# Optimization experiments

Measured on AMD Instinct MI355X. Metric: run time of the kernel, lower is better.

Reference implementation:

```python
import jax, jax.numpy as jnp
import numpy as np

D = 300   # hidden dim (Linear(300,300))
L = 160   # seq len, forced by W3 = Linear(160,1)


def _linear(x, W, b):
    # torch Linear: x @ W.T + b, W is (out, in)
    return jnp.matmul(x, W.T) + b


def setup_inputs() -> dict:
    key = jax.random.key(0)
    ks = jax.random.split(key, 16)
    B = 1024
    s = 1.0 / np.sqrt(D)
    inp = {
        'T_feature': jax.random.normal(ks[0], (B, L, D), jnp.float32),
        'CD_feature': jax.random.normal(ks[1], (B, L, D), jnp.float32),
        'Wproj': jax.random.normal(ks[2], (D, D), jnp.float32) * s,
        'bproj': jnp.zeros((D,), jnp.float32),
        'WqT_w': jax.random.normal(ks[3], (D, D), jnp.float32) * s,
        'WqT_b': jnp.zeros((D,), jnp.float32),
        'WqCD_w': jax.random.normal(ks[4], (D, D), jnp.float32) * s,
        'WqCD_b': jnp.zeros((D,), jnp.float32),
        'WkT_w': jax.random.normal(ks[5], (D, D), jnp.float32) * s,
        'WkT_b': jnp.zeros((D,), jnp.float32),
        'WkCD_w': jax.random.normal(ks[6], (D, D), jnp.float32) * s,
        'WkCD_b': jnp.zeros((D,), jnp.float32),
        'W3_w': jax.random.normal(ks[7], (1, L), jnp.float32) * (1.0 / np.sqrt(L)),
        'W3_b': jnp.zeros((1,), jnp.float32),
    }
    return inp


def reference(T_feature, CD_feature, Wproj, bproj, WqT_w, WqT_b, WqCD_w, WqCD_b,
              WkT_w, WkT_b, WkCD_w, WkCD_b, W3_w, W3_b):
    sqrt_d = jnp.sqrt(jnp.float32(D))
    proj_T = _linear(T_feature, Wproj, bproj)     # (B, L, D)
    proj_CD = _linear(CD_feature, Wproj, bproj)   # (B, L, D)

    # N_tensor @ proj_T is just the mean over tokens (weights 1/Len)
    mean_T = jnp.mean(proj_T, axis=1, keepdims=True)          # (B, 1, D)
    qT = _linear(mean_T, WqT_w, WqT_b)                        # (B, 1, D)
    kT = _linear(proj_T, WkT_w, WkT_b)                        # (B, L, D)
    alphaT = jnp.einsum('bqd,bkd->bqk', qT, kT) / sqrt_d      # (B, 1, L)
    ZT = jax.nn.sigmoid(alphaT)

    qCD = _linear(proj_CD, WqCD_w, WqCD_b)                    # (B, L, D)
    kCD = _linear(proj_CD, WkCD_w, WkCD_b)                    # (B, L, D)
    alphaCD = jnp.einsum('bqd,bkd->bqk', qCD, kCD) / sqrt_d   # (B, L, L)
    ZCD = jax.nn.sigmoid(alphaCD)

    # The per-token loop+cat is a plain broadcast multiply: Mt[:,i,:] = ZCD[:,i,:] * ZT[:,0,:]
    Mt = ZCD * ZT                                             # (B, L, L)
    alpha_f = jax.nn.softmax(_linear(Mt, W3_w, W3_b), axis=1) # (B, L, 1)

    # Second loop is a per-token scalar scale: HCD[:,i,:] = alpha_f[:,i,0] * proj_CD[:,i,:]
    HCD = alpha_f * proj_CD                                   # (B, L, D)
    return (proj_T, HCD)
```

## Files before the change

kernel.cpp:

```cpp
#include <hip/hip_runtime.h>
#include <hip/hip_bf16.h>


typedef __attribute__((ext_vector_type(8))) short short8;
typedef __attribute__((ext_vector_type(4))) float f32x4;

#define DP 320

__device__ __forceinline__ unsigned short f2bf(float x) {
  unsigned int u = __builtin_bit_cast(unsigned int, x);
  u += 0x7FFFu + ((u >> 16) & 1u);
  return (unsigned short)(u >> 16);
}
__device__ __forceinline__ float bf2f(unsigned short h) {
  unsigned int u = ((unsigned int)h) << 16;
  return __builtin_bit_cast(float, u);
}
__device__ __forceinline__ void gload16(const void* g, void* l) {
  __builtin_amdgcn_global_load_lds(
      (const __attribute__((address_space(1))) unsigned int*)g,
      (__attribute__((address_space(3))) unsigned int*)l, 16, 0, 0);
}
__device__ __forceinline__ float sigm(float x) { return 1.0f / (1.0f + __expf(-x)); }
__device__ __forceinline__ size_t baddr(int n, int k) {
  return (size_t)(k >> 6) * 20480 + (size_t)(n >> 4) * 1024 + ((k >> 5) & 1) * 512 +
         ((((k >> 3) & 3) << 4) | (n & 15)) * 8 + (k & 7);
}
__device__ __forceinline__ size_t aaddr(size_t r, int k) {
  return ((r >> 4) * 5 + (k >> 6)) * 1024 + ((k >> 5) & 1) * 512 +
         ((((k >> 3) & 3) << 4) | (r & 15)) * 8 + (k & 7);
}

__global__ __launch_bounds__(320)
void prep1_k(const float* __restrict__ W,
             const float* __restrict__ WqCD_w, const float* __restrict__ WqCD_b,
             const float* __restrict__ WkCD_w, const float* __restrict__ WkCD_b,
             const float* __restrict__ WqT_w, const float* __restrict__ WqT_b,
             const float* __restrict__ WkT_w, const float* __restrict__ WkT_b,
             unsigned short* __restrict__ Wb, float* __restrict__ Wt,
             unsigned short* __restrict__ MaugT, float* __restrict__ Maug_f,
             float* __restrict__ Pmat, float isd) {
  const int x = blockIdx.x, c = threadIdx.x;
  if (x < 320) {
    const int n = x;
    unsigned short v = (n < 300 && c < 300) ? f2bf(W[n * 300 + c]) : (unsigned short)0;
    Wb[baddr(n, c)] = v;
    if (n < 300 && c < 300) Wt[c * 304 + n] = W[n * 300 + c];
  } else if (x < 640) {
    const int n = x - 320;
    float v = 0.f;
    if (n <= 300 && c <= 300) {
      for (int o = 0; o < 300; ++o) {
        float a = (c < 300) ? WqCD_w[o * 300 + c] : WqCD_b[o];
        float b = (n < 300) ? WkCD_w[o * 300 + n] : WkCD_b[o];
        v += a * b;
      }
      v *= isd;
    }
    MaugT[baddr(n, c)] = f2bf(v);
    Maug_f[n * DP + c] = v;
  } else {
    const int n = x - 640;
    float v = 0.f;
    if (n <= 300 && c <= 300) {
      for (int o = 0; o < 300; ++o) {
        float a = (c < 300) ? WkT_w[o * 300 + c] : WkT_b[o];
        float b = (n < 300) ? WqT_w[o * 300 + n] : WqT_b[o];
        v += a * b;
      }
      v *= isd;
    }
    Pmat[n * DP + c] = v;
  }
}

__global__ __launch_bounds__(320)
void gh_k(const float* __restrict__ Maug_f, const float* __restrict__ W,
          const float* __restrict__ bproj, unsigned short* __restrict__ Gswz,
          float* __restrict__ h) {
  const int n = blockIdx.x, o = threadIdx.x;
  float v = 0.f;
  if (o < 300) {
    for (int c = 0; c < 300; ++c) v += Maug_f[n * DP + c] * W[c * 300 + o];
  } else if (o == 300) {
    float s = 0.f;
    for (int c = 0; c < 300; ++c) s += Maug_f[n * DP + c] * bproj[c];
    h[n] = s + Maug_f[n * DP + 300];
  }
  if (o > 300 && o == 301) {  }
  Gswz[baddr(n, o)] = (o < 300) ? f2bf(v) : (unsigned short)0;
  if (o == 300 && n == 0) {  }
}

__global__ __launch_bounds__(256)
void cvt_k(const float* __restrict__ T, const float* __restrict__ CD,
           unsigned short* __restrict__ Abf) {
  unsigned idx = blockIdx.x * 256 + threadIdx.x;
  if (idx >= 20480u * 640u) return;
  unsigned row16 = idx / 640u, rem = idx - row16 * 640u;
  int kc = rem >> 7, kk = (rem >> 6) & 1, lane = rem & 63;
  int lr = lane & 15, hi = lane >> 4;
  size_t row = (size_t)row16 * 16 + lr;
  int col0 = kc * 64 + kk * 32 + hi * 8;
  const float* base = (row < 163840u) ? T + row * 300 : CD + (row - 163840u) * 300;
  short8 h;
  if (col0 + 8 <= 300) {
    f32x4 x0 = *(const f32x4*)(base + col0), x1 = *(const f32x4*)(base + col0 + 4);
#pragma unroll
    for (int j = 0; j < 4; ++j) { h[j] = (short)f2bf(x0[j]); h[j + 4] = (short)f2bf(x1[j]); }
  } else {
#pragma unroll
    for (int j = 0; j < 8; ++j) {
      int c = col0 + j;
      h[j] = (short)((c < 300) ? f2bf(base[c]) : (unsigned short)0);
    }
  }
  *(short8*)(Abf + (size_t)idx * 8) = h;
}

__global__ __launch_bounds__(256, 2)
void gemm_k(const unsigned short* __restrict__ A0, const unsigned short* __restrict__ A1,
            const unsigned short* __restrict__ A2,
            const unsigned short* __restrict__ B01, const unsigned short* __restrict__ B2,
            const float* __restrict__ bias, const float* __restrict__ ybias,
            float* __restrict__ Of, unsigned short* __restrict__ pCDout,
            unsigned short* __restrict__ Yout, int mode_base) {
  __shared__ __align__(16) unsigned short Bs[2][20480];
  const int tid = threadIdx.x, wid = tid >> 6, lane = tid & 63;
  const int lr = lane & 15, hi = lane >> 4;
  const int mode = mode_base + blockIdx.y;
  const unsigned short* __restrict__ A = (mode == 0) ? A0 : (mode == 1) ? A1 : A2;
  const unsigned short* __restrict__ Bm = (mode == 2) ? B2 : B01;
  const size_t m0 = (size_t)blockIdx.x * 128;
  const size_t rt0 = (m0 >> 4) + wid * 2;

  f32x4 acc[2][20];
#pragma unroll
  for (int i = 0; i < 2; ++i)
#pragma unroll
    for (int j = 0; j < 20; ++j) acc[i][j] = (f32x4){0.f, 0.f, 0.f, 0.f};

  auto stageB = [&](int buf, int kc) {
#pragma unroll
    for (int it = 0; it < 10; ++it) {
      int idx = it * 256 + tid;
      gload16(Bm + (size_t)kc * 20480 + (size_t)idx * 8, (char*)Bs[buf] + idx * 16);
    }
  };
  short8 af[2][2][2];
  auto loadA = [&](short8 (&dst)[2][2], int kc) {
#pragma unroll
    for (int mf = 0; mf < 2; ++mf)
#pragma unroll
      for (int kk = 0; kk < 2; ++kk)
        dst[mf][kk] = *(const short8*)(A + ((rt0 + mf) * 5 + kc) * 1024 + kk * 512 + lane * 8);
  };

  stageB(0, 0);
  loadA(af[0], 0);
  __syncthreads();
#pragma unroll
  for (int kc = 0; kc < 5; ++kc) {
    const int cur = kc & 1;
    if (kc < 4) { stageB(cur ^ 1, kc + 1); loadA(af[cur ^ 1], kc + 1); }
#pragma unroll
    for (int kk = 0; kk < 2; ++kk)
#pragma unroll
      for (int nf = 0; nf < 20; ++nf) {
        short8 bb = *(const short8*)&Bs[cur][nf * 1024 + kk * 512 + lane * 8];
#pragma unroll
        for (int mf = 0; mf < 2; ++mf)
          acc[mf][nf] = __builtin_amdgcn_mfma_f32_16x16x32_bf16(af[cur][mf][kk], bb, acc[mf][nf], 0, 0, 0);
      }
    __syncthreads();
  }

#pragma unroll
  for (int mf = 0; mf < 2; ++mf)
#pragma unroll
    for (int nf = 0; nf < 20; ++nf) {
      const int col = nf * 16 + lr;
      const float bv = (mode == 2) ? (ybias ? ybias[col] : 0.f)
                                   : ((col < 300) ? bias[col] : 0.f);
      const size_t row16o = rt0 + mf;
#pragma unroll
      for (int r = 0; r < 4; ++r) {
        const size_t row = (row16o << 4) + hi * 4 + r;
        float v = acc[mf][nf][r] + bv;
        if (mode == 0) {
          if (col < 300) Of[row * 300 + col] = v;
        } else {
          unsigned short u = (mode == 2) ? f2bf(v)
                           : (col < 300) ? f2bf(v)
                           : (col == 300) ? f2bf(1.0f) : (unsigned short)0;
          unsigned short* dst = (mode == 1) ? pCDout : Yout;
          dst[(row16o * 5 + (col >> 6)) * 1024 + ((col >> 5) & 1) * 512 +
              ((((col >> 3) & 3) << 4) | (hi * 4 + r)) * 8 + (col & 7)] = u;
        }
      }
    }
}

__global__ __launch_bounds__(320)
void gate2_k(const float* __restrict__ T, const float* __restrict__ Pmat,
             const float* __restrict__ W, const float* __restrict__ Wt,
             const float* __restrict__ bproj, float* __restrict__ ZT) {
  __shared__ float mt[304];
  __shared__ float maug[304];
  __shared__ float vv[304];
  __shared__ float wt[304];
  __shared__ float cpr;
  const int b = blockIdx.x, t = threadIdx.x;
  const int wid = t >> 6, lane = t & 63;
  const float* Tb = T + (size_t)b * 48000;
  if (t < 300) {
    float s = 0.f;
#pragma unroll 4
    for (int l = 0; l < 160; ++l) s += Tb[l * 300 + t];
    mt[t] = s * (1.0f / 160.0f);
  }
  __syncthreads();
  if (t < 304) {
    if (t < 300) {
      float s = 0.f;
      for (int o = 0; o < 300; ++o) s += Wt[o * 304 + t] * mt[o];
      maug[t] = s + bproj[t];
    } else maug[t] = (t == 300) ? 1.f : 0.f;
  }
  __syncthreads();
  if (t < 304) {
    float s = 0.f;
    if (t <= 300) for (int a = 0; a <= 300; ++a) s += Pmat[a * DP + t] * maug[a];
    vv[t] = s;
  }
  __syncthreads();
  if (t < 304) {
    if (t < 300) {
      float s = 0.f;
      for (int c = 0; c < 300; ++c) s += vv[c] * W[c * 300 + t];
      wt[t] = s;
    } else {
      wt[t] = 0.f;
      if (t == 300) {
        float s = 0.f;
        for (int c = 0; c < 300; ++c) s += vv[c] * bproj[c];
        cpr = s + vv[300];
      }
    }
  }
  __syncthreads();
  for (int j = wid * 32; j < wid * 32 + 32; ++j) {
    const float* row = Tb + j * 300;
    float s = 0.f;
    for (int c = lane; c < 300; c += 64) s += wt[c] * row[c];
#pragma unroll
    for (int m = 1; m < 64; m <<= 1) s += __shfl_xor(s, m, 64);
    if (lane == 0) ZT[b * 160 + j] = sigm(s + cpr);
  }
}

__global__ __launch_bounds__(640)
void finale_k(const unsigned short* __restrict__ Yg, const unsigned short* __restrict__ Pg,
              const float* __restrict__ ZT, const float* __restrict__ W3w,
              float* __restrict__ out) {
  __shared__ __align__(16) unsigned short Ps[51200];
  __shared__ float t_arr[160];
  __shared__ float s_arr[160];
  __shared__ float red0;
  const int b = blockIdx.x, tid = threadIdx.x, wid = tid >> 6, lane = tid & 63;
  const int lr = lane & 15, hi = lane >> 4;
  const unsigned short* Pb = Pg + (size_t)b * 51200;
  const unsigned short* Yb = Yg + (size_t)b * 51200;

  if (tid < 160) t_arr[tid] = ZT[b * 160 + tid] * W3w[tid];

  auto stageP = [&](int kc) {
#pragma unroll
    for (int it = 0; it < 2; ++it) {
      int idx = it * 640 + tid;
      int r16 = idx >> 7, rem = idx & 127;
      gload16(Pb + ((size_t)r16 * 5 + kc) * 1024 + (size_t)rem * 8,
              (char*)Ps + ((size_t)kc * 10240 + (size_t)idx * 8) * 2);
    }
  };
  short8 yf[2][2];
  auto loadY = [&](short8 (&dst)[2], int kc) {
#pragma unroll
    for (int kk = 0; kk < 2; ++kk)
      dst[kk] = *(const short8*)(Yb + ((size_t)wid * 5 + kc) * 1024 + kk * 512 + lane * 8);
  };

  f32x4 acc[10];
#pragma unroll
  for (int j = 0; j < 10; ++j) acc[j] = (f32x4){0.f, 0.f, 0.f, 0.f};

  stageP(0);
  loadY(yf[0], 0);
  __syncthreads();
#pragma unroll
  for (int kc = 0; kc < 5; ++kc) {
    const int cur = kc & 1;
    if (kc < 4) { stageP(kc + 1); loadY(yf[cur ^ 1], kc + 1); }
#pragma unroll
    for (int kk = 0; kk < 2; ++kk)
#pragma unroll
      for (int nf = 0; nf < 10; ++nf) {
        short8 bb = *(const short8*)&Ps[kc * 10240 + nf * 1024 + kk * 512 + lane * 8];
        acc[nf] = __builtin_amdgcn_mfma_f32_16x16x32_bf16(yf[cur][kk], bb, acc[nf], 0, 0, 0);
      }
    __syncthreads();
  }

  float pp[4];
#pragma unroll
  for (int r = 0; r < 4; ++r) {
    float s = 0.f;
#pragma unroll
    for (int nf = 0; nf < 10; ++nf) s += sigm(acc[nf][r]) * t_arr[nf * 16 + lr];
    pp[r] = s;
  }
#pragma unroll
  for (int m = 1; m < 16; m <<= 1)
#pragma unroll
    for (int r = 0; r < 4; ++r) pp[r] += __shfl_xor(pp[r], m, 64);
  if (lr == 0) {
#pragma unroll
    for (int r = 0; r < 4; ++r) s_arr[wid * 16 + hi * 4 + r] = pp[r];
  }
  __syncthreads();
  if (wid == 0) {
    float v0 = s_arr[lane], v1 = s_arr[lane + 64];
    float v2 = (lane < 32) ? s_arr[lane + 128] : -3.0e38f;
    float mx = fmaxf(fmaxf(v0, v1), v2);
#pragma unroll
    for (int m = 1; m < 64; m <<= 1) mx = fmaxf(mx, __shfl_xor(mx, m, 64));
    float e0 = __expf(v0 - mx), e1 = __expf(v1 - mx);
    float e2 = (lane < 32) ? __expf(v2 - mx) : 0.f;
    s_arr[lane] = e0; s_arr[lane + 64] = e1;
    if (lane < 32) s_arr[lane + 128] = e2;
    float sm = e0 + e1 + e2;
#pragma unroll
    for (int m = 1; m < 64; m <<= 1) sm += __shfl_xor(sm, m, 64);
    if (lane == 0) red0 = 1.0f / sm;
  }
  __syncthreads();
  const float inv = red0;
  float* ob = out + (size_t)b * 48000;
#pragma unroll
  for (int it = 0; it < 10; ++it) {
    int idx = it * 640 + tid;
    int i = idx / 40, g = idx - i * 40;
    int c0 = g * 8;
    if (c0 < 300) {
      short8 pv = *(const short8*)&Ps[(g >> 3) * 10240 + (i >> 4) * 1024 +
                                      ((g >> 2) & 1) * 512 + ((((g & 3) << 4) | (i & 15)) * 8)];
      float sc = s_arr[i] * inv;
      if (c0 + 8 <= 300) {
        f32x4 o0, o1;
#pragma unroll
        for (int j = 0; j < 4; ++j) { o0[j] = sc * bf2f((unsigned short)pv[j]); o1[j] = sc * bf2f((unsigned short)pv[j + 4]); }
        *(f32x4*)(ob + (size_t)i * 300 + c0) = o0;
        *(f32x4*)(ob + (size_t)i * 300 + c0 + 4) = o1;
      } else {
#pragma unroll
        for (int j = 0; j < 8; ++j) {
          int c = c0 + j;
          if (c < 300) ob[(size_t)i * 300 + c] = sc * bf2f((unsigned short)pv[j]);
        }
      }
    }
  }
}

extern "C" void kernel_launch(void* const* d_in, const int* in_sizes, int n_in,
                              void* d_out, int out_size, void* d_ws, size_t ws_size,
                              hipStream_t stream) {
  (void)in_sizes; (void)n_in; (void)out_size;
  const float* T      = (const float*)d_in[0];
  const float* CD     = (const float*)d_in[1];
  const float* Wproj  = (const float*)d_in[2];
  const float* bproj  = (const float*)d_in[3];
  const float* WqT_w  = (const float*)d_in[4];
  const float* WqT_b  = (const float*)d_in[5];
  const float* WqCD_w = (const float*)d_in[6];
  const float* WqCD_b = (const float*)d_in[7];
  const float* WkT_w  = (const float*)d_in[8];
  const float* WkT_b  = (const float*)d_in[9];
  const float* WkCD_w = (const float*)d_in[10];
  const float* WkCD_b = (const float*)d_in[11];
  const float* W3_w   = (const float*)d_in[12];

  char* ws = (char*)d_ws;
  size_t off = 0;
  auto alloc = [&](size_t bytes) { void* p = ws + off; off = (off + bytes + 255) & ~(size_t)255; return p; };
  unsigned short* Wb     = (unsigned short*)alloc((size_t)DP * DP * 2);
  unsigned short* MaugT  = (unsigned short*)alloc((size_t)DP * DP * 2);
  unsigned short* Gswz   = (unsigned short*)alloc((size_t)DP * DP * 2);
  float* Maug_f = (float*)alloc((size_t)DP * DP * 4);
  float* Pmat   = (float*)alloc((size_t)DP * DP * 4);
  float* Wt     = (float*)alloc((size_t)304 * 304 * 4);
  float* hb     = (float*)alloc((size_t)DP * 4);
  float* ZT     = (float*)alloc((size_t)1024 * 160 * 4);
  unsigned short* Abf = (unsigned short*)alloc((size_t)327680 * DP * 2);
  unsigned short* AbfCD = Abf + (size_t)163840 * DP;

  const size_t half = (size_t)163840 * DP * 2;
  const bool big = (ws_size > off) && ((ws_size - off) >= 2 * half + 1024);
  unsigned short* pCDg = big ? (unsigned short*)alloc(half) : AbfCD;
  unsigned short* Yg   = big ? (unsigned short*)alloc(half) : Abf;

  float* projT = (float*)d_out;
  float* HCD   = (float*)d_out + (size_t)49152000;

  const float isd = 1.0f / sqrtf(300.0f);

  prep1_k<<<dim3(960), dim3(320), 0, stream>>>(Wproj, WqCD_w, WqCD_b, WkCD_w, WkCD_b,
                                               WqT_w, WqT_b, WkT_w, WkT_b,
                                               Wb, Wt, MaugT, Maug_f, Pmat, isd);
  gh_k<<<dim3(320), dim3(320), 0, stream>>>(Maug_f, Wproj, bproj, Gswz, hb);
  cvt_k<<<dim3(51200), dim3(256), 0, stream>>>(T, CD, Abf);
  gate2_k<<<dim3(1024), dim3(320), 0, stream>>>(T, Pmat, Wproj, Wt, bproj, ZT);

  if (big) {
    gemm_k<<<dim3(1280, 3), dim3(256), 0, stream>>>(Abf, AbfCD, AbfCD, Wb, Gswz,
                                                    bproj, hb, projT, pCDg, Yg, 0);
  } else {
    gemm_k<<<dim3(1280, 2), dim3(256), 0, stream>>>(Abf, AbfCD, nullptr, Wb, nullptr,
                                                    bproj, nullptr, projT, pCDg, nullptr, 0);
    gemm_k<<<dim3(1280, 1), dim3(256), 0, stream>>>(nullptr, nullptr, pCDg, Wb, MaugT,
                                                    bproj, nullptr, projT, nullptr, Yg, 2);
  }
  finale_k<<<dim3(1024), dim3(640), 0, stream>>>(Yg, pCDg, ZT, W3_w, HCD);
}
```

Before: 688.8 us.

## Fuse fp32-to-bf16 conversion into GEMM and retile to 512-thread 2D warp grid

Removes the separate cvt_k pass that wrote a bf16 swizzled copy of T and CD, and the gh_k kernel. The GEMM now loads fp32 rows directly, converts them to bf16 in registers and writes them into a double-buffered LDS A tile. The GEMM also moves from 256 threads with 2x20 fragments per warp to 512 threads in a 2x4 warp grid with 4x5 fragments. The Y GEMM is always run in a second pass from pCD with MaugT, and the gh_k/Gswz shortcut is dropped. This removes a large bf16 write and read round trip, at the cost of more in-kernel conversion and an extra dependent launch.

```diff
diff --git a/kernel.cpp b/kernel.cpp
--- a/kernel.cpp
+++ b/kernel.cpp
@@ -38,8 +38,8 @@
              const float* __restrict__ WqT_w, const float* __restrict__ WqT_b,
              const float* __restrict__ WkT_w, const float* __restrict__ WkT_b,
              unsigned short* __restrict__ Wb, float* __restrict__ Wt,
-             unsigned short* __restrict__ MaugT, float* __restrict__ Maug_f,
-             float* __restrict__ Pmat, float isd) {
+             unsigned short* __restrict__ MaugT, float* __restrict__ Pmat,
+             float isd) {
   const int x = blockIdx.x, c = threadIdx.x;
   if (x < 320) {
     const int n = x;
@@ -58,7 +58,6 @@
       v *= isd;
     }
     MaugT[baddr(n, c)] = f2bf(v);
-    Maug_f[n * DP + c] = v;
   } else {
     const int n = x - 640;
     float v = 0.f;
@@ -74,131 +73,134 @@
   }
 }
 
-__global__ __launch_bounds__(320)
-void gh_k(const float* __restrict__ Maug_f, const float* __restrict__ W,
-          const float* __restrict__ bproj, unsigned short* __restrict__ Gswz,
-          float* __restrict__ h) {
-  const int n = blockIdx.x, o = threadIdx.x;
-  float v = 0.f;
-  if (o < 300) {
-    for (int c = 0; c < 300; ++c) v += Maug_f[n * DP + c] * W[c * 300 + o];
-  } else if (o == 300) {
-    float s = 0.f;
-    for (int c = 0; c < 300; ++c) s += Maug_f[n * DP + c] * bproj[c];
-    h[n] = s + Maug_f[n * DP + 300];
-  }
-  if (o > 300 && o == 301) {  }
-  Gswz[baddr(n, o)] = (o < 300) ? f2bf(v) : (unsigned short)0;
-  if (o == 300 && n == 0) {  }
-}
-
-__global__ __launch_bounds__(256)
-void cvt_k(const float* __restrict__ T, const float* __restrict__ CD,
-           unsigned short* __restrict__ Abf) {
-  unsigned idx = blockIdx.x * 256 + threadIdx.x;
-  if (idx >= 20480u * 640u) return;
-  unsigned row16 = idx / 640u, rem = idx - row16 * 640u;
-  int kc = rem >> 7, kk = (rem >> 6) & 1, lane = rem & 63;
-  int lr = lane & 15, hi = lane >> 4;
-  size_t row = (size_t)row16 * 16 + lr;
-  int col0 = kc * 64 + kk * 32 + hi * 8;
-  const float* base = (row < 163840u) ? T + row * 300 : CD + (row - 163840u) * 300;
-  short8 h;
-  if (col0 + 8 <= 300) {
-    f32x4 x0 = *(const f32x4*)(base + col0), x1 = *(const f32x4*)(base + col0 + 4);
-#pragma unroll
-    for (int j = 0; j < 4; ++j) { h[j] = (short)f2bf(x0[j]); h[j + 4] = (short)f2bf(x1[j]); }
-  } else {
-#pragma unroll
-    for (int j = 0; j < 8; ++j) {
-      int c = col0 + j;
-      h[j] = (short)((c < 300) ? f2bf(base[c]) : (unsigned short)0);
-    }
-  }
-  *(short8*)(Abf + (size_t)idx * 8) = h;
-}
-
-__global__ __launch_bounds__(256, 2)
-void gemm_k(const unsigned short* __restrict__ A0, const unsigned short* __restrict__ A1,
-            const unsigned short* __restrict__ A2,
-            const unsigned short* __restrict__ B01, const unsigned short* __restrict__ B2,
-            const float* __restrict__ bias, const float* __restrict__ ybias,
+__global__ __launch_bounds__(512)
+void gemm_k(const float* __restrict__ Tf, const float* __restrict__ CDf,
+            const unsigned short* __restrict__ Ah,
+            const unsigned short* __restrict__ B01,
+            const unsigned short* __restrict__ B2,
+            const float* __restrict__ bias,
             float* __restrict__ Of, unsigned short* __restrict__ pCDout,
             unsigned short* __restrict__ Yout, int mode_base) {
+  __shared__ __align__(16) unsigned short As[2][8192];
   __shared__ __align__(16) unsigned short Bs[2][20480];
   const int tid = threadIdx.x, wid = tid >> 6, lane = tid & 63;
   const int lr = lane & 15, hi = lane >> 4;
+  const int wr = wid >> 2, wc = wid & 3;
   const int mode = mode_base + blockIdx.y;
-  const unsigned short* __restrict__ A = (mode == 0) ? A0 : (mode == 1) ? A1 : A2;
+  const size_t m0 = (size_t)blockIdx.x * 128;
   const unsigned short* __restrict__ Bm = (mode == 2) ? B2 : B01;
-  const size_t m0 = (size_t)blockIdx.x * 128;
-  const size_t rt0 = (m0 >> 4) + wid * 2;
-
-  f32x4 acc[2][20];
-#pragma unroll
-  for (int i = 0; i < 2; ++i)
-#pragma unroll
-    for (int j = 0; j < 20; ++j) acc[i][j] = (f32x4){0.f, 0.f, 0.f, 0.f};
-
+  const float* __restrict__ Af = (mode == 0) ? Tf : CDf;
+
+  f32x4 acc[4][5];
+#pragma unroll
+  for (int i = 0; i < 4; ++i)
+#pragma unroll
+    for (int j = 0; j < 5; ++j) acc[i][j] = (f32x4){0.f, 0.f, 0.f, 0.f};
+
+  f32x4 ar[4];
+  auto loadA = [&](int kc) {
+#pragma unroll
+    for (int u = 0; u < 2; ++u) {
+      const int unit = tid * 2 + u;
+      const int row = unit >> 3, cg = unit & 7;
+      const int col0 = kc * 64 + cg * 8;
+      const float* p = Af + (m0 + row) * 300 + col0;
+      if (col0 + 8 <= 300) {
+        ar[u * 2] = *(const f32x4*)p;
+        ar[u * 2 + 1] = *(const f32x4*)(p + 4);
+      } else {
+#pragma unroll
+        for (int j = 0; j < 4; ++j) {
+          ar[u * 2][j] = (col0 + j < 300) ? p[j] : 0.f;
+          ar[u * 2 + 1][j] = (col0 + 4 + j < 300) ? p[4 + j] : 0.f;
+        }
+      }
+    }
+  };
+  auto writeA = [&](int buf) {
+#pragma unroll
+    for (int u = 0; u < 2; ++u) {
+      const int unit = tid * 2 + u;
+      const int row = unit >> 3, cg = unit & 7;
+      short8 h;
+#pragma unroll
+      for (int j = 0; j < 4; ++j) {
+        h[j] = (short)f2bf(ar[u * 2][j]);
+        h[j + 4] = (short)f2bf(ar[u * 2 + 1][j]);
+      }
+      *(short8*)&As[buf][(size_t)(row >> 4) * 1024 + (size_t)(cg >> 2) * 512 +
+                         ((((cg & 3) << 4) | (row & 15)) * 8)] = h;
+    }
+  };
+  auto stageA2 = [&](int buf, int kc) {
+#pragma unroll
+    for (int it = 0; it < 2; ++it) {
+      int idx = it * 512 + tid;
+      gload16(Ah + (((m0 >> 4) + (idx >> 7)) * 5 + kc) * 1024 + (size_t)(idx & 127) * 8,
+              (char*)As[buf] + (size_t)idx * 16);
+    }
+  };
   auto stageB = [&](int buf, int kc) {
 #pragma unroll
-    for (int it = 0; it < 10; ++it) {
-      int idx = it * 256 + tid;
-      gload16(Bm + (size_t)kc * 20480 + (size_t)idx * 8, (char*)Bs[buf] + idx * 16);
-    }
-  };
-  short8 af[2][2][2];
-  auto loadA = [&](short8 (&dst)[2][2], int kc) {
-#pragma unroll
-    for (int mf = 0; mf < 2; ++mf)
-#pragma unroll
-      for (int kk = 0; kk < 2; ++kk)
-        dst[mf][kk] = *(const short8*)(A + ((rt0 + mf) * 5 + kc) * 1024 + kk * 512 + lane * 8);
-  };
-
-  stageB(0, 0);
-  loadA(af[0], 0);
-  __syncthreads();
-#pragma unroll
+    for (int it = 0; it < 5; ++it) {
+      int idx = it * 512 + tid;
+      gload16(Bm + (size_t)kc * 20480 + (size_t)idx * 8, (char*)Bs[buf] + (size_t)idx * 16);
+    }
+  };
+
+  if (mode < 2) { loadA(0); stageB(0, 0); writeA(0); }
+  else { stageA2(0, 0); stageB(0, 0); }
+  __syncthreads();
+
   for (int kc = 0; kc < 5; ++kc) {
     const int cur = kc & 1;
-    if (kc < 4) { stageB(cur ^ 1, kc + 1); loadA(af[cur ^ 1], kc + 1); }
-#pragma unroll
-    for (int kk = 0; kk < 2; ++kk)
-#pragma unroll
-      for (int nf = 0; nf < 20; ++nf) {
-        short8 bb = *(const short8*)&Bs[cur][nf * 1024 + kk * 512 + lane * 8];
-#pragma unroll
-        for (int mf = 0; mf < 2; ++mf)
-          acc[mf][nf] = __builtin_amdgcn_mfma_f32_16x16x32_bf16(af[cur][mf][kk], bb, acc[mf][nf], 0, 0, 0);
-      }
+    if (kc < 4) {
+      if (mode < 2) loadA(kc + 1);
+      else stageA2(cur ^ 1, kc + 1);
+      stageB(cur ^ 1, kc + 1);
+    }
+#pragma unroll
+    for (int kk = 0; kk < 2; ++kk) {
+      short8 a[4], b[5];
+#pragma unroll
+      for (int mf = 0; mf < 4; ++mf)
+        a[mf] = *(const short8*)&As[cur][(size_t)(wr * 4 + mf) * 1024 + kk * 512 + lane * 8];
+#pragma unroll
+      for (int nf = 0; nf < 5; ++nf)
+        b[nf] = *(const short8*)&Bs[cur][(size_t)(wc * 5 + nf) * 1024 + kk * 512 + lane * 8];
+#pragma unroll
+      for (int mf = 0; mf < 4; ++mf)
+#pragma unroll
+        for (int nf = 0; nf < 5; ++nf)
+          acc[mf][nf] = __builtin_amdgcn_mfma_f32_16x16x32_bf16(a[mf], b[nf], acc[mf][nf], 0, 0, 0);
+    }
+    if (kc < 4 && mode < 2) writeA(cur ^ 1);
     __syncthreads();
   }
 
 #pragma unroll
-  for (int mf = 0; mf < 2; ++mf)
-#pragma unroll
-    for (int nf = 0; nf < 20; ++nf) {
-      const int col = nf * 16 + lr;
-      const float bv = (mode == 2) ? (ybias ? ybias[col] : 0.f)
-                                   : ((col < 300) ? bias[col] : 0.f);
-      const size_t row16o = rt0 + mf;
+  for (int mf = 0; mf < 4; ++mf) {
+    const size_t rowb = m0 + wr * 64 + mf * 16 + hi * 4;
+#pragma unroll
+    for (int nf = 0; nf < 5; ++nf) {
+      const int col = wc * 80 + nf * 16 + lr;
+      const float bv = (mode < 2) ? ((col < 300) ? bias[col] : 0.f) : 0.f;
 #pragma unroll
       for (int r = 0; r < 4; ++r) {
-        const size_t row = (row16o << 4) + hi * 4 + r;
+        const size_t rw = rowb + r;
         float v = acc[mf][nf][r] + bv;
         if (mode == 0) {
-          if (col < 300) Of[row * 300 + col] = v;
+          if (col < 300) Of[rw * 300 + col] = v;
+        } else if (mode == 1) {
+          unsigned short u = (col < 300) ? f2bf(v)
+                           : ((col == 300) ? f2bf(1.0f) : (unsigned short)0);
+          pCDout[aaddr(rw, col)] = u;
         } else {
-          unsigned short u = (mode == 2) ? f2bf(v)
-                           : (col < 300) ? f2bf(v)
-                           : (col == 300) ? f2bf(1.0f) : (unsigned short)0;
-          unsigned short* dst = (mode == 1) ? pCDout : Yout;
-          dst[(row16o * 5 + (col >> 6)) * 1024 + ((col >> 5) & 1) * 512 +
-              ((((col >> 3) & 3) << 4) | (hi * 4 + r)) * 8 + (col & 7)] = u;
+          Yout[aaddr(rw, col)] = f2bf(v);
         }
       }
     }
+  }
 }
 
 __global__ __launch_bounds__(320)
@@ -375,7 +377,7 @@
 extern "C" void kernel_launch(void* const* d_in, const int* in_sizes, int n_in,
                               void* d_out, int out_size, void* d_ws, size_t ws_size,
                               hipStream_t stream) {
-  (void)in_sizes; (void)n_in; (void)out_size;
+  (void)in_sizes; (void)n_in; (void)out_size; (void)ws_size;
   const float* T      = (const float*)d_in[0];
   const float* CD     = (const float*)d_in[1];
   const float* Wproj  = (const float*)d_in[2];
@@ -393,21 +395,13 @@
   char* ws = (char*)d_ws;
   size_t off = 0;
   auto alloc = [&](size_t bytes) { void* p = ws + off; off = (off + bytes + 255) & ~(size_t)255; return p; };
-  unsigned short* Wb     = (unsigned short*)alloc((size_t)DP * DP * 2);
-  unsigned short* MaugT  = (unsigned short*)alloc((size_t)DP * DP * 2);
-  unsigned short* Gswz   = (unsigned short*)alloc((size_t)DP * DP * 2);
-  float* Maug_f = (float*)alloc((size_t)DP * DP * 4);
-  float* Pmat   = (float*)alloc((size_t)DP * DP * 4);
-  float* Wt     = (float*)alloc((size_t)304 * 304 * 4);
-  float* hb     = (float*)alloc((size_t)DP * 4);
-  float* ZT     = (float*)alloc((size_t)1024 * 160 * 4);
-  unsigned short* Abf = (unsigned short*)alloc((size_t)327680 * DP * 2);
-  unsigned short* AbfCD = Abf + (size_t)163840 * DP;
-
-  const size_t half = (size_t)163840 * DP * 2;
-  const bool big = (ws_size > off) && ((ws_size - off) >= 2 * half + 1024);
-  unsigned short* pCDg = big ? (unsigned short*)alloc(half) : AbfCD;
-  unsigned short* Yg   = big ? (unsigned short*)alloc(half) : Abf;
+  unsigned short* Wb    = (unsigned short*)alloc((size_t)DP * DP * 2);
+  unsigned short* MaugT = (unsigned short*)alloc((size_t)DP * DP * 2);
+  float* Pmat = (float*)alloc((size_t)DP * DP * 4);
+  float* Wt   = (float*)alloc((size_t)304 * 304 * 4);
+  float* ZT   = (float*)alloc((size_t)1024 * 160 * 4);
+  unsigned short* pCDg = (unsigned short*)alloc((size_t)163840 * DP * 2);
+  unsigned short* Yg   = (unsigned short*)alloc((size_t)163840 * DP * 2);
 
   float* projT = (float*)d_out;
   float* HCD   = (float*)d_out + (size_t)49152000;
@@ -416,19 +410,11 @@
 
   prep1_k<<<dim3(960), dim3(320), 0, stream>>>(Wproj, WqCD_w, WqCD_b, WkCD_w, WkCD_b,
                                                WqT_w, WqT_b, WkT_w, WkT_b,
-                                               Wb, Wt, MaugT, Maug_f, Pmat, isd);
-  gh_k<<<dim3(320), dim3(320), 0, stream>>>(Maug_f, Wproj, bproj, Gswz, hb);
-  cvt_k<<<dim3(51200), dim3(256), 0, stream>>>(T, CD, Abf);
+                                               Wb, Wt, MaugT, Pmat, isd);
+  gemm_k<<<dim3(1280, 2), dim3(512), 0, stream>>>(T, CD, nullptr, Wb, nullptr,
+                                                  bproj, projT, pCDg, nullptr, 0);
+  gemm_k<<<dim3(1280, 1), dim3(512), 0, stream>>>(nullptr, nullptr, pCDg, nullptr, MaugT,
+                                                  nullptr, nullptr, nullptr, Yg, 2);
   gate2_k<<<dim3(1024), dim3(320), 0, stream>>>(T, Pmat, Wproj, Wt, bproj, ZT);
-
-  if (big) {
-    gemm_k<<<dim3(1280, 3), dim3(256), 0, stream>>>(Abf, AbfCD, AbfCD, Wb, Gswz,
-                                                    bproj, hb, projT, pCDg, Yg, 0);
-  } else {
-    gemm_k<<<dim3(1280, 2), dim3(256), 0, stream>>>(Abf, AbfCD, nullptr, Wb, nullptr,
-                                                    bproj, nullptr, projT, pCDg, nullptr, 0);
-    gemm_k<<<dim3(1280, 1), dim3(256), 0, stream>>>(nullptr, nullptr, pCDg, Wb, MaugT,
-                                                    bproj, nullptr, projT, nullptr, Yg, 2);
-  }
   finale_k<<<dim3(1024), dim3(640), 0, stream>>>(Yg, pCDg, ZT, W3_w, HCD);
 }
```

Measured after the change: 669.8 us. 2.8% less time.
